# Kernel tuning notes

Measured on AMD Instinct MI355X. Metric: run time of the kernel, lower is better.

Reference implementation:

```python
import jax, jax.numpy as jnp
import numpy as np
from itertools import product

C0, C1, C_IN, C_OUT = 16, 32, 1, 32
GRID = 768

def _enc(c):
    # injective int64 hash of 3D integer coords (values in [-4, 2043])
    return ((c[:, 0] + 4) * 2048 + (c[:, 1] + 4)) * 2048 + (c[:, 2] + 4)

def _build_km(coords, offsets):
    # kernel map for a stride-1 conv on one coordinate set:
    # per kernel offset o, pairs (in_idx, out_idx) with coords[in] == coords[out] + o
    N = coords.shape[0]
    keys = _enc(coords)
    order = np.argsort(keys)
    skeys = keys[order]
    ins, outs = [], []
    for o in offsets:
        qk = _enc(coords + np.asarray(o, np.int64))
        pos = np.searchsorted(skeys, qk)
        posc = np.clip(pos, 0, N - 1)
        valid = skeys[posc] == qk
        ins.append(order[posc[valid]].astype(np.int32))
        outs.append(np.nonzero(valid)[0].astype(np.int32))
    P = max(len(a) for a in ins)
    km_in = np.full((len(offsets), P), N, np.int32)   # pad -> zero row of x
    km_out = np.full((len(offsets), P), N, np.int32)  # pad -> dropped out row
    for k in range(len(offsets)):
        km_in[k, :len(ins[k])] = ins[k]
        km_out[k, :len(outs[k])] = outs[k]
    return km_in, km_out

def setup_inputs() -> dict:
    # voxelized surface heightfield: realistic sparse 3D point cloud occupancy
    xs, ys = np.meshgrid(np.arange(GRID), np.arange(GRID), indexing='ij')
    z = np.round(40.0 * np.sin(xs / 24.0) + 40.0 * np.cos(ys / 24.0)).astype(np.int64) + 128
    coords0 = np.stack([xs.ravel(), ys.ravel(), z.ravel()], 1).astype(np.int64)
    n0 = coords0.shape[0]
    offs27 = list(product((-1, 0, 1), repeat=3))
    km0_in, km0_out = _build_km(coords0, offs27)

    # stride-2 kernel-2 downsample: out coord = floor(c/2), offset = c mod 2
    u2 = coords0 // 2
    coords1, inv = np.unique(u2, axis=0, return_inverse=True)
    inv = inv.reshape(-1)
    n1 = coords1.shape[0]
    o = coords0 - 2 * u2
    kk = o[:, 0] * 4 + o[:, 1] * 2 + o[:, 2]
    ins, outs = [], []
    for k in range(8):
        m = np.nonzero(kk == k)[0]
        ins.append(m.astype(np.int32))
        outs.append(inv[m].astype(np.int32))
    P = max(len(a) for a in ins)
    kmd_in = np.full((8, P), n0, np.int32)
    kmd_out = np.full((8, P), n1, np.int32)
    for k in range(8):
        kmd_in[k, :len(ins[k])] = ins[k]
        kmd_out[k, :len(outs[k])] = outs[k]

    km1_in, km1_out = _build_km(coords1, offs27)

    key = jax.random.key(0)
    ks = jax.random.split(key, 6)
    w = lambda k, sh: jax.random.normal(k, sh, jnp.float32) * 0.1
    z32 = lambda c: jnp.zeros((c,), jnp.float32)
    return dict(
        in_feats=jnp.ones((n0, C_IN), jnp.float32),
        W_first=w(ks[0], (27, C_IN, C0)), b_first=z32(C0),
        W_pre=w(ks[1], (27, C0, C0)), b_pre=z32(C0),
        W_down=w(ks[2], (8, C0, C1)), b_down=z32(C1),
        W_r0=w(ks[3], (27, C1, C1)), b_r0=z32(C1),
        W_r1=w(ks[4], (27, C1, C1)), b_r1=z32(C1),
        W_fin=w(ks[5], (27, C1, C_OUT)), b_fin=z32(C_OUT),
        km0_in=jnp.asarray(km0_in), km0_out=jnp.asarray(km0_out),
        kmd_in=jnp.asarray(kmd_in), kmd_out=jnp.asarray(kmd_out),
        km1_in=jnp.asarray(km1_in), km1_out=jnp.asarray(km1_out),
        n1=int(n1),
    )

def _sparse_conv(x, W, b, km_in, km_out, n_out):
    # gather-GEMM-scatter sparse conv: out[j] += x[i] @ W[k] over pairs of offset k
    xp = jnp.concatenate([x, jnp.zeros((1, x.shape[1]), x.dtype)], 0)
    out = jnp.zeros((n_out + 1, W.shape[-1]), x.dtype)
    for k in range(W.shape[0]):  # static small loop over kernel offsets
        out = out.at[km_out[k]].add(xp[km_in[k]] @ W[k])
    return out[:n_out] + b

def reference(in_feats, W_first, b_first, W_pre, b_pre, W_down, b_down,
              W_r0, b_r0, W_r1, b_r1, W_fin, b_fin,
              km0_in, km0_out, kmd_in, kmd_out, km1_in, km1_out, n1):
    n0 = in_feats.shape[0]
    relu = jax.nn.relu
    # first_block: 3^3 conv + relu
    x = relu(_sparse_conv(in_feats, W_first, b_first, km0_in, km0_out, n0))
    cached = x  # cached_feature_list[0] (use_skip_connection=False)
    # blocks[0]: conv3x3 + relu, stride-2 downsample conv + relu
    x = relu(_sparse_conv(x, W_pre, b_pre, km0_in, km0_out, n0))
    x = relu(_sparse_conv(x, W_down, b_down, kmd_in, kmd_out, n1))
    # ResBlock
    r = relu(_sparse_conv(x, W_r0, b_r0, km1_in, km1_out, n1))
    r = _sparse_conv(r, W_r1, b_r1, km1_in, km1_out, n1)
    x = r + x
    # final conv (act=None)
    out = _sparse_conv(x, W_fin, b_fin, km1_in, km1_out, n1)
    return (out, cached)
```

## Files before the change

### kernel.cpp

```cpp
#include <hip/hip_runtime.h>


#define TPB 256

typedef __attribute__((ext_vector_type(8))) short short8;
typedef __attribute__((ext_vector_type(4))) float floatx4;

static __device__ __forceinline__ unsigned short f2b(float f) {
    union { float f; unsigned u; } v; v.f = f;
    unsigned r = v.u + 0x7fffu + ((v.u >> 16) & 1u);
    return (unsigned short)(r >> 16);
}
static __device__ __forceinline__ float b2f(unsigned short h) {
    union { unsigned u; float f; } v; v.u = ((unsigned)h) << 16;
    return v.f;
}

__global__ void fill_i32v(int* __restrict__ p, long long n4, int val) {
    long long i = (long long)blockIdx.x * blockDim.x + threadIdx.x;
    if (i < n4) ((int4*)p)[i] = make_int4(val, val, val, val);
}

__global__ void scatter_tab(const int* __restrict__ km_in,
                            const int* __restrict__ km_out,
                            int* __restrict__ tab, long long rowcap, long long P,
                            long long total) {
    long long t = (long long)blockIdx.x * blockDim.x + threadIdx.x;
    if (t >= total) return;
    long long k = t / P;
    int o = km_out[t];
    tab[k * rowcap + o] = km_in[t];
}

__global__ void zero_pads(unsigned short* a, unsigned short* b, unsigned short* c,
                          unsigned short* d, unsigned short* e) {
    int t = threadIdx.x;
    if (t < 16) a[t] = 0;
    else if (t < 32) b[t - 16] = 0;
    else if (t < 64) c[t - 32] = 0;
    else if (t < 96) d[t - 64] = 0;
    else if (t < 128) e[t - 96] = 0;
}

__global__ void pack_w32(const float* __restrict__ W, unsigned short* __restrict__ Wp,
                         int K) {
    int t = blockIdx.x * blockDim.x + threadIdx.x;
    if (t >= K * 1024) return;
    int j = t & 7, n = (t >> 3) & 31, q = (t >> 8) & 3, k = t >> 10;
    Wp[t] = f2b(W[(k * 32 + q * 8 + j) * 32 + n]);
}

__global__ void pack_w16(const float* __restrict__ W, unsigned short* __restrict__ Wp,
                         int K2, int COUT, int Ksrc) {
    int t = blockIdx.x * blockDim.x + threadIdx.x;
    if (t >= K2 * 4 * COUT * 8) return;
    int j = t & 7;
    int r = t >> 3;
    int n = r % COUT; r /= COUT;
    int q = r & 3;
    int k2 = r >> 2;
    int ks = 2 * k2 + (q >> 1);
    int cin = (q & 1) * 8 + j;
    float v = (ks < Ksrc) ? W[(ks * 16 + cin) * COUT + n] : 0.f;
    Wp[t] = f2b(v);
}

__global__ __launch_bounds__(TPB) void conv_first_k(
    const float* __restrict__ xin, const float* __restrict__ W,
    const float* __restrict__ b, const int* __restrict__ tab, long long rowcap,
    int n0, float* __restrict__ outf, unsigned short* __restrict__ outb) {
    int j = blockIdx.x * blockDim.x + threadIdx.x;
    if (j >= n0) return;
    float acc[16];
#pragma unroll
    for (int c = 0; c < 16; ++c) acc[c] = b[c];
#pragma unroll
    for (int k = 0; k < 27; ++k) {
        int idx = tab[(long long)k * rowcap + j];
        int cidx = idx < n0 ? idx : 0;
        float v = xin[cidx];
        v = idx < n0 ? v : 0.f;
        const float* Wk = W + k * 16;
#pragma unroll
        for (int c = 0; c < 16; ++c) acc[c] = fmaf(v, Wk[c], acc[c]);
    }
    float* orow = outf + (long long)j * 16;
    unsigned short* brow = outb + (long long)j * 16;
#pragma unroll
    for (int c = 0; c < 16; ++c) {
        float v = fmaxf(acc[c], 0.f);
        orow[c] = v;
        brow[c] = f2b(v);
    }
}

template <int CIN, int COUT, int STEPS, bool RELU, bool RES, bool WF32, bool WB16>
__global__ __launch_bounds__(TPB, 4) void conv_mfma(
    const unsigned short* __restrict__ xb,
    const unsigned short* __restrict__ Wp,
    const float* __restrict__ bias,
    const int* __restrict__ tab, long long rowcap, int n_out,
    const unsigned short* __restrict__ resb,
    float* __restrict__ outf, unsigned short* __restrict__ outb) {
    constexpr int NT = COUT / 16;
    int wid = (blockIdx.x * (int)blockDim.x + (int)threadIdx.x) >> 6;
    int lane = threadIdx.x & 63;
    int m = lane & 15, q = lane >> 4;
    long long j0 = (long long)wid * 64;
    if (j0 >= n_out) return;
    floatx4 acc[4][NT];
#pragma unroll
    for (int t = 0; t < 4; ++t)
#pragma unroll
        for (int nt = 0; nt < NT; ++nt) acc[t][nt] = floatx4{0.f, 0.f, 0.f, 0.f};
#pragma unroll
    for (int s = 0; s < STEPS; ++s) {
        int ks, coff;
        if (CIN == 32) { ks = s; coff = q * 8; }
        else { ks = 2 * s + (q >> 1); coff = (q & 1) * 8; }
        const int* trow = tab + (long long)ks * rowcap + j0 + m;
        int idx[4];
#pragma unroll
        for (int t = 0; t < 4; ++t) idx[t] = trow[16 * t];
        short8 b0 = *(const short8*)(Wp + (((s * 4 + q) * COUT) + m) * 8);
        short8 b1;
        if (NT == 2) b1 = *(const short8*)(Wp + (((s * 4 + q) * COUT) + 16 + m) * 8);
#pragma unroll
        for (int t = 0; t < 4; ++t) {
            short8 a = *(const short8*)(xb + (long long)idx[t] * CIN + coff);
            acc[t][0] = __builtin_amdgcn_mfma_f32_16x16x32_bf16(a, b0, acc[t][0], 0, 0, 0);
            if (NT == 2)
                acc[t][1] = __builtin_amdgcn_mfma_f32_16x16x32_bf16(a, b1, acc[t][1], 0, 0, 0);
        }
    }
    float bs[2];
    bs[0] = bias[m];
    if (NT == 2) bs[1] = bias[16 + m];
#pragma unroll
    for (int t = 0; t < 4; ++t) {
#pragma unroll
        for (int u = 0; u < 4; ++u) {
            long long r = j0 + 16 * t + q * 4 + u;
            if (r < n_out) {
#pragma unroll
                for (int nt = 0; nt < NT; ++nt) {
                    float v = acc[t][nt][u] + bs[nt];
                    if (RES) v += b2f(resb[r * COUT + nt * 16 + m]);
                    if (RELU) v = fmaxf(v, 0.f);
                    if (WF32) outf[r * COUT + nt * 16 + m] = v;
                    if (WB16) outb[r * COUT + nt * 16 + m] = f2b(v);
                }
            }
        }
    }
}

static inline unsigned nblk(long long n, int b) { return (unsigned)((n + b - 1) / b); }
static inline size_t align64(size_t x) { return (x + 63) & ~(size_t)63; }

extern "C" void kernel_launch(void* const* d_in, const int* in_sizes, int n_in_cnt,
                              void* d_out, int out_size, void* d_ws, size_t ws_size,
                              hipStream_t stream) {
    const float* in_feats = (const float*)d_in[0];
    const float* W_first = (const float*)d_in[1];
    const float* b_first = (const float*)d_in[2];
    const float* W_pre   = (const float*)d_in[3];
    const float* b_pre   = (const float*)d_in[4];
    const float* W_down  = (const float*)d_in[5];
    const float* b_down  = (const float*)d_in[6];
    const float* W_r0    = (const float*)d_in[7];
    const float* b_r0    = (const float*)d_in[8];
    const float* W_r1    = (const float*)d_in[9];
    const float* b_r1    = (const float*)d_in[10];
    const float* W_fin   = (const float*)d_in[11];
    const float* b_fin   = (const float*)d_in[12];
    const int* km0_in  = (const int*)d_in[13];
    const int* km0_out = (const int*)d_in[14];
    const int* kmd_in  = (const int*)d_in[15];
    const int* kmd_out = (const int*)d_in[16];
    const int* km1_in  = (const int*)d_in[17];
    const int* km1_out = (const int*)d_in[18];

    const int n0 = in_sizes[0];
    const int n1 = (out_size - 16 * n0) / 32;
    const long long P0 = in_sizes[13] / 27;
    const long long Pd = in_sizes[15] / 8;
    const long long P1 = in_sizes[17] / 27;

    const long long rc0 = ((n0 + 64) / 64) * 64;
    const long long rc1 = ((n1 + 64) / 64) * 64;

    float* out_lo = (float*)d_out;
    float* cached = out_lo + (size_t)n1 * 32;

    char* base = (char*)d_ws;
    size_t off = 0;
    auto alloc = [&](size_t bytes) { void* p = base + off; off = align64(off + bytes); return p; };
    int* t0 = (int*)alloc(sizeof(int) * 28 * rc0);
    int* t1 = (int*)alloc(sizeof(int) * 27 * rc1);
    int* td = (int*)alloc(sizeof(int) * 8 * rc1);
    unsigned short* c0b   = (unsigned short*)alloc(sizeof(short) * 16 * (n0 + 1));
    unsigned short* x0pre = (unsigned short*)alloc(sizeof(short) * 16 * (n0 + 1));
    unsigned short* x1a   = (unsigned short*)alloc(sizeof(short) * 32 * (n1 + 1));
    unsigned short* x1b   = (unsigned short*)alloc(sizeof(short) * 32 * (n1 + 1));
    unsigned short* x1c   = (unsigned short*)alloc(sizeof(short) * 32 * (n1 + 1));
    unsigned short* wp_pre  = (unsigned short*)alloc(sizeof(short) * 14 * 4 * 16 * 8);
    unsigned short* wp_down = (unsigned short*)alloc(sizeof(short) * 4 * 4 * 32 * 8);
    unsigned short* wp_r0   = (unsigned short*)alloc(sizeof(short) * 27 * 1024);
    unsigned short* wp_r1   = (unsigned short*)alloc(sizeof(short) * 27 * 1024);
    unsigned short* wp_fin  = (unsigned short*)alloc(sizeof(short) * 27 * 1024);
    (void)ws_size; (void)n_in_cnt;

    fill_i32v<<<nblk(28 * rc0 / 4, TPB), TPB, 0, stream>>>(t0, 28 * rc0 / 4, n0);
    fill_i32v<<<nblk(27 * rc1 / 4, TPB), TPB, 0, stream>>>(t1, 27 * rc1 / 4, n1);
    fill_i32v<<<nblk(8 * rc1 / 4, TPB), TPB, 0, stream>>>(td, 8 * rc1 / 4, n0);
    scatter_tab<<<nblk(27 * P0, TPB), TPB, 0, stream>>>(km0_in, km0_out, t0, rc0, P0, 27 * P0);
    scatter_tab<<<nblk(27 * P1, TPB), TPB, 0, stream>>>(km1_in, km1_out, t1, rc1, P1, 27 * P1);
    scatter_tab<<<nblk(8 * Pd, TPB), TPB, 0, stream>>>(kmd_in, kmd_out, td, rc1, Pd, 8 * Pd);

    pack_w16<<<nblk(14 * 4 * 16 * 8, TPB), TPB, 0, stream>>>(W_pre, wp_pre, 14, 16, 27);
    pack_w16<<<nblk(4 * 4 * 32 * 8, TPB), TPB, 0, stream>>>(W_down, wp_down, 4, 32, 8);
    pack_w32<<<nblk(27 * 1024, TPB), TPB, 0, stream>>>(W_r0, wp_r0, 27);
    pack_w32<<<nblk(27 * 1024, TPB), TPB, 0, stream>>>(W_r1, wp_r1, 27);
    pack_w32<<<nblk(27 * 1024, TPB), TPB, 0, stream>>>(W_fin, wp_fin, 27);
    zero_pads<<<1, 160, 0, stream>>>(c0b + (size_t)n0 * 16, x0pre + (size_t)n0 * 16,
                                     x1a + (size_t)n1 * 32, x1b + (size_t)n1 * 32,
                                     x1c + (size_t)n1 * 32);

    conv_first_k<<<nblk(n0, TPB), TPB, 0, stream>>>(in_feats, W_first, b_first, t0, rc0,
                                                    n0, cached, c0b);
    const long long th0 = (long long)nblk(n0, 64) * 64;
    const long long th1 = (long long)nblk(n1, 64) * 64;
    conv_mfma<16, 16, 14, true, false, false, true><<<nblk(th0, TPB), TPB, 0, stream>>>(
        c0b, wp_pre, b_pre, t0, rc0, n0, nullptr, nullptr, x0pre);
    conv_mfma<16, 32, 4, true, false, false, true><<<nblk(th1, TPB), TPB, 0, stream>>>(
        x0pre, wp_down, b_down, td, rc1, n1, nullptr, nullptr, x1a);
    conv_mfma<32, 32, 27, true, false, false, true><<<nblk(th1, TPB), TPB, 0, stream>>>(
        x1a, wp_r0, b_r0, t1, rc1, n1, nullptr, nullptr, x1b);
    conv_mfma<32, 32, 27, false, true, false, true><<<nblk(th1, TPB), TPB, 0, stream>>>(
        x1b, wp_r1, b_r1, t1, rc1, n1, x1a, nullptr, x1c);
    conv_mfma<32, 32, 27, false, false, true, false><<<nblk(th1, TPB), TPB, 0, stream>>>(
        x1c, wp_fin, b_fin, t1, rc1, n1, nullptr, out_lo, nullptr);
}
```

Measured before the change: 520.0 us.

## Software-pipeline gathers in MFMA sparse conv and use memset for table init

Restructures the MFMA conv loop to prefetch kernel-map indices two steps ahead and the gathered feature rows one step ahead, so global gather latency overlaps with the MFMA work of the current step. The neighbour tables are now filled with 0xFF through hipMemsetAsync instead of a custom fill kernel, and invalid (negative) indices are clamped in-kernel to the zero pad row. Block size for the conv kernels drops to 128 threads and the occupancy hint is removed. The extra prefetch buffers raise register pressure, which can reduce occupancy.

```diff
diff --git a/kernel.cpp b/kernel.cpp
--- a/kernel.cpp
+++ b/kernel.cpp
@@ -2,6 +2,7 @@
 
 
 #define TPB 256
+#define TPC 128
 
 typedef __attribute__((ext_vector_type(8))) short short8;
 typedef __attribute__((ext_vector_type(4))) float floatx4;
@@ -14,11 +15,6 @@
 static __device__ __forceinline__ float b2f(unsigned short h) {
     union { unsigned u; float f; } v; v.u = ((unsigned)h) << 16;
     return v.f;
-}
-
-__global__ void fill_i32v(int* __restrict__ p, long long n4, int val) {
-    long long i = (long long)blockIdx.x * blockDim.x + threadIdx.x;
-    if (i < n4) ((int4*)p)[i] = make_int4(val, val, val, val);
 }
 
 __global__ void scatter_tab(const int* __restrict__ km_in,
@@ -77,9 +73,10 @@
 #pragma unroll
     for (int k = 0; k < 27; ++k) {
         int idx = tab[(long long)k * rowcap + j];
-        int cidx = idx < n0 ? idx : 0;
+        bool ok = (unsigned)idx < (unsigned)n0;
+        int cidx = ok ? idx : 0;
         float v = xin[cidx];
-        v = idx < n0 ? v : 0.f;
+        v = ok ? v : 0.f;
         const float* Wk = W + k * 16;
 #pragma unroll
         for (int c = 0; c < 16; ++c) acc[c] = fmaf(v, Wk[c], acc[c]);
@@ -95,11 +92,11 @@
 }
 
 template <int CIN, int COUT, int STEPS, bool RELU, bool RES, bool WF32, bool WB16>
-__global__ __launch_bounds__(TPB, 4) void conv_mfma(
+__global__ __launch_bounds__(TPC) void conv_mfma(
     const unsigned short* __restrict__ xb,
     const unsigned short* __restrict__ Wp,
     const float* __restrict__ bias,
-    const int* __restrict__ tab, long long rowcap, int n_out,
+    const int* __restrict__ tab, long long rowcap, int n_in, int n_out,
     const unsigned short* __restrict__ resb,
     float* __restrict__ outf, unsigned short* __restrict__ outb) {
     constexpr int NT = COUT / 16;
@@ -108,31 +105,60 @@
     int m = lane & 15, q = lane >> 4;
     long long j0 = (long long)wid * 64;
     if (j0 >= n_out) return;
+
     floatx4 acc[4][NT];
 #pragma unroll
     for (int t = 0; t < 4; ++t)
 #pragma unroll
         for (int nt = 0; nt < NT; ++nt) acc[t][nt] = floatx4{0.f, 0.f, 0.f, 0.f};
+
+    const int coff = (CIN == 32) ? q * 8 : (q & 1) * 8;
+
+    auto load_idx = [&](int s, int (&dst)[4]) {
+        int ks = (CIN == 32) ? s : 2 * s + (q >> 1);
+        const int* trow = tab + (long long)ks * rowcap + j0 + m;
+#pragma unroll
+        for (int t = 0; t < 4; ++t) {
+            int v = trow[16 * t];
+            dst[t] = ((unsigned)v < (unsigned)n_in) ? v : n_in;
+        }
+    };
+    auto gather = [&](const int (&src)[4], short8 (&dst)[4]) {
+#pragma unroll
+        for (int t = 0; t < 4; ++t)
+            dst[t] = *(const short8*)(xb + (long long)src[t] * CIN + coff);
+    };
+
+    int idxB[4];
+    short8 aCur[4];
+    {
+        int idxA[4];
+        load_idx(0, idxA);
+        if (STEPS > 1) load_idx(1, idxB);
+        gather(idxA, aCur);
+    }
 #pragma unroll
     for (int s = 0; s < STEPS; ++s) {
-        int ks, coff;
-        if (CIN == 32) { ks = s; coff = q * 8; }
-        else { ks = 2 * s + (q >> 1); coff = (q & 1) * 8; }
-        const int* trow = tab + (long long)ks * rowcap + j0 + m;
-        int idx[4];
-#pragma unroll
-        for (int t = 0; t < 4; ++t) idx[t] = trow[16 * t];
+        int idxN[4];
+        short8 aN[4];
+        if (s + 2 < STEPS) load_idx(s + 2, idxN);
+        if (s + 1 < STEPS) gather(idxB, aN);
         short8 b0 = *(const short8*)(Wp + (((s * 4 + q) * COUT) + m) * 8);
         short8 b1;
         if (NT == 2) b1 = *(const short8*)(Wp + (((s * 4 + q) * COUT) + 16 + m) * 8);
 #pragma unroll
         for (int t = 0; t < 4; ++t) {
-            short8 a = *(const short8*)(xb + (long long)idx[t] * CIN + coff);
-            acc[t][0] = __builtin_amdgcn_mfma_f32_16x16x32_bf16(a, b0, acc[t][0], 0, 0, 0);
+            acc[t][0] = __builtin_amdgcn_mfma_f32_16x16x32_bf16(aCur[t], b0, acc[t][0], 0, 0, 0);
             if (NT == 2)
-                acc[t][1] = __builtin_amdgcn_mfma_f32_16x16x32_bf16(a, b1, acc[t][1], 0, 0, 0);
-        }
-    }
+                acc[t][1] = __builtin_amdgcn_mfma_f32_16x16x32_bf16(aCur[t], b1, acc[t][1], 0, 0, 0);
+        }
+#pragma unroll
+        for (int t = 0; t < 4; ++t) {
+            if (s + 1 < STEPS) aCur[t] = aN[t];
+            if (s + 2 < STEPS) idxB[t] = idxN[t];
+        }
+    }
+
     float bs[2];
     bs[0] = bias[m];
     if (NT == 2) bs[1] = bias[16 + m];
@@ -211,9 +237,9 @@
     unsigned short* wp_fin  = (unsigned short*)alloc(sizeof(short) * 27 * 1024);
     (void)ws_size; (void)n_in_cnt;
 
-    fill_i32v<<<nblk(28 * rc0 / 4, TPB), TPB, 0, stream>>>(t0, 28 * rc0 / 4, n0);
-    fill_i32v<<<nblk(27 * rc1 / 4, TPB), TPB, 0, stream>>>(t1, 27 * rc1 / 4, n1);
-    fill_i32v<<<nblk(8 * rc1 / 4, TPB), TPB, 0, stream>>>(td, 8 * rc1 / 4, n0);
+    hipMemsetAsync(t0, 0xFF, sizeof(int) * 28 * rc0, stream);
+    hipMemsetAsync(t1, 0xFF, sizeof(int) * 27 * rc1, stream);
+    hipMemsetAsync(td, 0xFF, sizeof(int) * 8 * rc1, stream);
     scatter_tab<<<nblk(27 * P0, TPB), TPB, 0, stream>>>(km0_in, km0_out, t0, rc0, P0, 27 * P0);
     scatter_tab<<<nblk(27 * P1, TPB), TPB, 0, stream>>>(km1_in, km1_out, t1, rc1, P1, 27 * P1);
     scatter_tab<<<nblk(8 * Pd, TPB), TPB, 0, stream>>>(kmd_in, kmd_out, td, rc1, Pd, 8 * Pd);
@@ -229,16 +255,15 @@
 
     conv_first_k<<<nblk(n0, TPB), TPB, 0, stream>>>(in_feats, W_first, b_first, t0, rc0,
                                                     n0, cached, c0b);
-    const long long th0 = (long long)nblk(n0, 64) * 64;
-    const long long th1 = (long long)nblk(n1, 64) * 64;
-    conv_mfma<16, 16, 14, true, false, false, true><<<nblk(th0, TPB), TPB, 0, stream>>>(
-        c0b, wp_pre, b_pre, t0, rc0, n0, nullptr, nullptr, x0pre);
-    conv_mfma<16, 32, 4, true, false, false, true><<<nblk(th1, TPB), TPB, 0, stream>>>(
-        x0pre, wp_down, b_down, td, rc1, n1, nullptr, nullptr, x1a);
-    conv_mfma<32, 32, 27, true, false, false, true><<<nblk(th1, TPB), TPB, 0, stream>>>(
-        x1a, wp_r0, b_r0, t1, rc1, n1, nullptr, nullptr, x1b);
-    conv_mfma<32, 32, 27, false, true, false, true><<<nblk(th1, TPB), TPB, 0, stream>>>(
-        x1b, wp_r1, b_r1, t1, rc1, n1, x1a, nullptr, x1c);
-    conv_mfma<32, 32, 27, false, false, true, false><<<nblk(th1, TPB), TPB, 0, stream>>>(
-        x1c, wp_fin, b_fin, t1, rc1, n1, nullptr, out_lo, nullptr);
-}
+    const long long w0 = nblk(n0, 64), w1 = nblk(n1, 64);
+    conv_mfma<16, 16, 14, true, false, false, true><<<nblk(w0 * 64, TPC), TPC, 0, stream>>>(
+        c0b, wp_pre, b_pre, t0, rc0, n0, n0, nullptr, nullptr, x0pre);
+    conv_mfma<16, 32, 4, true, false, false, true><<<nblk(w1 * 64, TPC), TPC, 0, stream>>>(
+        x0pre, wp_down, b_down, td, rc1, n0, n1, nullptr, nullptr, x1a);
+    conv_mfma<32, 32, 27, true, false, false, true><<<nblk(w1 * 64, TPC), TPC, 0, stream>>>(
+        x1a, wp_r0, b_r0, t1, rc1, n1, n1, nullptr, nullptr, x1b);
+    conv_mfma<32, 32, 27, false, true, false, true><<<nblk(w1 * 64, TPC), TPC, 0, stream>>>(
+        x1b, wp_r1, b_r1, t1, rc1, n1, n1, x1a, nullptr, x1c);
+    conv_mfma<32, 32, 27, false, false, true, false><<<nblk(w1 * 64, TPC), TPC, 0, stream>>>(
+        x1c, wp_fin, b_fin, t1, rc1, n1, n1, nullptr, out_lo, nullptr);
+}
```

Measured after the change: 514.3 us. No clear change (-1.1%).
